# Optimization experiments

Measured on AMD Instinct MI355X. Metric: run time of the kernel, lower is better.

Reference implementation:

```python
import jax, jax.numpy as jnp
import numpy as np

N_NODES = 2000
NEG_SLOPE = 0.01  # torch nn.LeakyReLU default


def setup_inputs() -> dict:
    key = jax.random.key(0)
    ks = jax.random.split(key, 7)
    B, T, N, F, E = 4, 12, N_NODES, 64, 32000
    state = jax.random.normal(ks[0], (B, T, N, F), dtype=jnp.float32)
    feature = jax.random.normal(ks[1], (N, F), dtype=jnp.float32)
    W = jax.random.normal(ks[2], (F, 2 * F), dtype=jnp.float32) / np.sqrt(2 * F)
    b = jnp.zeros((F,), dtype=jnp.float32)
    src = jax.random.randint(ks[3], (E,), 0, N)
    dst = jax.random.randint(ks[4], (E,), 0, N)
    dist = jax.random.uniform(ks[5], (E, 1), dtype=jnp.float32)
    return {"state": state, "feature": feature, "W": W, "b": b,
            "src": src, "dst": dst, "dist": dist}


def reference(state, feature, W, b, src, dst, dist):
    # state: [B,T,N,F] -> node-major [N,B,T,F] (matches unsqueeze/transpose/squeeze)
    s = jnp.moveaxis(state, 2, 0)                       # [N,B,T,F]
    s_src = s[src]                                      # [E,B,T,F] gather
    s_dst = s[dst]                                      # [E,B,T,F]
    h = jnp.concatenate([s_src, s_dst], axis=-1)        # [E,B,T,2F]
    alpha = jnp.einsum('ebtk,fk->ebtf', h, W) + b       # linear 2F->F
    alpha = jnp.where(alpha >= 0, alpha, NEG_SLOPE * alpha)  # LeakyReLU
    alpha = alpha * dist[:, None, None, :]              # dist [E,1] broadcast
    # segment softmax over incoming edges per destination node
    n = s.shape[0]
    m = jax.ops.segment_max(alpha, dst, num_segments=n)        # [N,B,T,F]
    ex = jnp.exp(alpha - m[dst])
    denom = jax.ops.segment_sum(ex, dst, num_segments=n)       # [N,B,T,F]
    w = ex / denom[dst]                                         # [E,B,T,F]
    new_state = jax.ops.segment_sum(w * s_src, dst, num_segments=n)
    new_state = jax.nn.relu(new_state)                  # [N,B,T,F]
    return jnp.moveaxis(new_state, 0, 2)                # [B,T,N,F]
```

## Files before the change

### kernel.cpp

```cpp
#include <hip/hip_runtime.h>
#include <hip/hip_bf16.h>
#include <hip/hip_fp16.h>
#include <math.h>


#define F_DIM 64
#define LOG2E 1.442695040888963f
#define CPAD 128
#define RSTRIDE 128

typedef _Float16 f16x8 __attribute__((ext_vector_type(8)));
typedef float f32x4 __attribute__((ext_vector_type(4)));


__global__ void hist_kernel(const int* __restrict__ dst, int* __restrict__ chunk_hist,
                            int E, int N) {
    __shared__ int h[2048];
    int t = threadIdx.x, c = blockIdx.x;
    for (int i = t; i < N; i += 256) h[i] = 0;
    __syncthreads();
    int e = c * 256 + t;
    if (e < E) atomicAdd(&h[dst[e]], 1);
    __syncthreads();
    for (int d = t; d < N; d += 256)
        chunk_hist[d * CPAD + c] = h[d];
}

__global__ void binscan_kernel(int* __restrict__ chunk_hist, int* __restrict__ counts,
                               int* __restrict__ esrc, float* __restrict__ edist,
                               int N, int C) {
    int wave = (blockIdx.x * blockDim.x + threadIdx.x) >> 6;
    int lane = threadIdx.x & 63;
    if (wave >= N) return;
    int* row = chunk_hist + wave * CPAD;
    int i0 = 2 * lane, i1 = 2 * lane + 1;
    int v0 = (i0 < C) ? row[i0] : 0;
    int v1 = (i1 < C) ? row[i1] : 0;
    int s = v0 + v1;
    int acc = s;
#pragma unroll
    for (int d = 1; d < 64; d <<= 1) {
        int up = __shfl_up(acc, d);
        if (lane >= d) acc += up;
    }
    int excl = acc - s;
    if (i0 < C) row[i0] = excl;
    if (i1 < C) row[i1] = excl + v0;
    int total = __shfl(acc, 63);
    if (lane == 63) counts[wave] = total;
    int* er = esrc + wave * RSTRIDE;
    float* dr = edist + wave * RSTRIDE;
    if (i0 >= total) { er[i0] = 0; dr[i0] = 0.f; }
    if (i1 >= total) { er[i1] = 0; dr[i1] = 0.f; }
}

__global__ void scatter2_kernel(const int* __restrict__ dst, const int* __restrict__ src,
                                const float* __restrict__ dist,
                                const int* __restrict__ chunk_hist,
                                int* __restrict__ esrc, float* __restrict__ edist, int E) {
    __shared__ int sdst[256];
    int t = threadIdx.x, c = blockIdx.x;
    int e = c * 256 + t;
    int d = (e < E) ? dst[e] : -1;
    sdst[t] = d;
    __syncthreads();
    if (e >= E) return;
    int cnt = 0;
#pragma unroll 8
    for (int j = 0; j < 256; j++)
        cnt += (j < t && sdst[j] == d) ? 1 : 0;
    int off = chunk_hist[d * CPAD + c] + cnt;
    if (off < RSTRIDE) {
        esrc[d * RSTRIDE + off] = src[e] << 8;
        edist[d * RSTRIDE + off] = dist[e] * LOG2E;
    }
}

__global__ __launch_bounds__(256) void gemm_pre_mfma(
    const float* __restrict__ state, const float* __restrict__ W,
    const float* __restrict__ bias,
    unsigned* __restrict__ PSh, float* __restrict__ P2B) {
    int tid = threadIdx.x;
    int wv = tid >> 6, lane = tid & 63;
    int l15 = lane & 15, l4 = lane >> 4;

    f16x8 bf[8][2];
#pragma unroll
    for (int ct = 0; ct < 8; ++ct) {
        int j = ct * 16 + l15;
        const float* wp = (j < 64) ? (W + j * 128) : (W + (j - 64) * 128 + 64);
#pragma unroll
        for (int kh = 0; kh < 2; ++kh) {
            const float* p = wp + kh * 32 + l4 * 8;
            float4 w0 = *(const float4*)p;
            float4 w1 = *(const float4*)(p + 4);
            f16x8 h;
            h[0] = (_Float16)w0.x; h[1] = (_Float16)w0.y;
            h[2] = (_Float16)w0.z; h[3] = (_Float16)w0.w;
            h[4] = (_Float16)w1.x; h[5] = (_Float16)w1.y;
            h[6] = (_Float16)w1.z; h[7] = (_Float16)w1.w;
            bf[ct][kh] = h;
        }
    }
    float b0 = bias[l15], b1 = bias[16 + l15], b2 = bias[32 + l15], b3 = bias[48 + l15];

    int r = blockIdx.x * 64 + wv * 16;

    const float* ap = state + (long)(r + l15) * 64 + l4 * 8;
    float4 a0 = *(const float4*)ap;
    float4 a1 = *(const float4*)(ap + 4);
    float4 a2 = *(const float4*)(ap + 32);
    float4 a3 = *(const float4*)(ap + 36);
    f16x8 af0, af1;
    af0[0] = (_Float16)a0.x; af0[1] = (_Float16)a0.y;
    af0[2] = (_Float16)a0.z; af0[3] = (_Float16)a0.w;
    af0[4] = (_Float16)a1.x; af0[5] = (_Float16)a1.y;
    af0[6] = (_Float16)a1.z; af0[7] = (_Float16)a1.w;
    af1[0] = (_Float16)a2.x; af1[1] = (_Float16)a2.y;
    af1[2] = (_Float16)a2.z; af1[3] = (_Float16)a2.w;
    af1[4] = (_Float16)a3.x; af1[5] = (_Float16)a3.y;
    af1[6] = (_Float16)a3.z; af1[7] = (_Float16)a3.w;

    f32x4 zero = {0.f, 0.f, 0.f, 0.f};
    f32x4 acc[8];
#pragma unroll
    for (int ct = 0; ct < 8; ++ct) {
        acc[ct] = __builtin_amdgcn_mfma_f32_16x16x32_f16(af0, bf[ct][0], zero, 0, 0, 0);
        acc[ct] = __builtin_amdgcn_mfma_f32_16x16x32_f16(af1, bf[ct][1], acc[ct], 0, 0, 0);
    }

    float bb0[4] = {b0, b1, b2, b3};
#pragma unroll
    for (int reg = 0; reg < 4; ++reg) {
        long rr = r + l4 * 4 + reg;
        const float* sp = state + rr * 64;
#pragma unroll
        for (int ct = 0; ct < 4; ++ct) {
            float sval = sp[ct * 16 + l15];
            __half2 h = __floats2half2_rn(acc[ct][reg], sval);
            PSh[rr * 64 + ct * 16 + l15] = *(unsigned*)&h;
        }
#pragma unroll
        for (int ct = 4; ct < 8; ++ct) {
            P2B[rr * 64 + (ct - 4) * 16 + l15] = acc[ct][reg] + bb0[ct - 4];
        }
    }
}


#define ECOMP(U, D, P2V, DEN, NUM)                                        \
    {                                                                     \
        float x;                                                          \
        asm("v_fma_mix_f32 %0, %1, %2, %3 op_sel:[0,0,0] op_sel_hi:[1,0,0]" \
            : "=v"(x) : "v"(U), "v"(fone), "v"(P2V));                     \
        float y0 = x * (D);                                               \
        float y1 = 0.01f * y0;                                            \
        float y = fmaxf(y0, y1);                                          \
        float p = __builtin_amdgcn_exp2f(y);                              \
        DEN += p;                                                         \
        asm("v_fma_mix_f32 %0, %1, %2, %0 op_sel:[0,1,0] op_sel_hi:[0,1,0]" \
            : "+v"(NUM) : "v"(p), "v"(U));                                \
    }

__global__ __launch_bounds__(384) void gat_kernel(
    const unsigned* __restrict__ PSh, const float* __restrict__ P2B,
    const int* __restrict__ esrc, const float* __restrict__ edist,
    const int* __restrict__ counts,
    float* __restrict__ out, int N, int NBT) {
    int b = blockIdx.x;
    int xcd = b & 7, pr = b >> 3;
    int w = threadIdx.x >> 6, f = threadIdx.x & 63;
    int bt = xcd * 6 + w;
    const char* PSb = (const char*)PSh + (size_t)bt * N * 256;
    int f4 = f << 2;
    int n0 = pr * 2;
    int cnt0 = counts[n0], cnt1 = counts[n0 + 1];
    const int4*   ep0 = (const int4*)(esrc + n0 * RSTRIDE);
    const float4* dp0 = (const float4*)(edist + n0 * RSTRIDE);
    const int4*   ep1 = ep0 + (RSTRIDE / 4);
    const float4* dp1 = dp0 + (RSTRIDE / 4);
    int ob0 = ((bt * N + n0) << 6) + f;
    float p2_0 = P2B[ob0];
    float p2_1 = P2B[ob0 + 64];
    unsigned z = *(const unsigned*)(PSb + f4);
    float zs = __half22float2(*(const __half2*)&z).y;
    float fone = 1.0f;
    int cm0 = (cnt0 > RSTRIDE) ? RSTRIDE : cnt0;
    int cm1 = (cnt1 > RSTRIDE) ? RSTRIDE : cnt1;
    int nq0 = (cm0 + 3) >> 2, nq1 = (cm1 + 3) >> 2;
    int nqm = (nq0 > nq1) ? nq0 : nq1;
    float denA0 = 0.f, denA1 = 0.f, numA0 = 0.f, numA1 = 0.f;
    float denB0 = 0.f, denB1 = 0.f, numB0 = 0.f, numB1 = 0.f;
    for (int q = 0; q < nqm; ++q) {
        int4   sa = ep0[q], sb = ep1[q];
        float4 da = dp0[q], db = dp1[q];
        unsigned a0 = *(const unsigned*)(PSb + sa.x + f4);
        unsigned a1 = *(const unsigned*)(PSb + sa.y + f4);
        unsigned a2 = *(const unsigned*)(PSb + sa.z + f4);
        unsigned a3 = *(const unsigned*)(PSb + sa.w + f4);
        unsigned b0 = *(const unsigned*)(PSb + sb.x + f4);
        unsigned b1 = *(const unsigned*)(PSb + sb.y + f4);
        unsigned b2 = *(const unsigned*)(PSb + sb.z + f4);
        unsigned b3 = *(const unsigned*)(PSb + sb.w + f4);
        ECOMP(a0, da.x, p2_0, denA0, numA0)
        ECOMP(b0, db.x, p2_1, denB0, numB0)
        ECOMP(a1, da.y, p2_0, denA1, numA1)
        ECOMP(b1, db.y, p2_1, denB1, numB1)
        ECOMP(a2, da.z, p2_0, denA0, numA0)
        ECOMP(b2, db.z, p2_1, denB0, numB0)
        ECOMP(a3, da.w, p2_0, denA1, numA1)
        ECOMP(b3, db.w, p2_1, denB1, numB1)
    }
    float npad0 = (float)((nqm << 2) - cm0);
    float npad1 = (float)((nqm << 2) - cm1);
    float o0 = (cnt0 > 0)
        ? fmaxf((numA0 + numA1 - npad0 * zs) / (denA0 + denA1 - npad0), 0.f) : 0.f;
    float o1 = (cnt1 > 0)
        ? fmaxf((numB0 + numB1 - npad1 * zs) / (denB0 + denB1 - npad1), 0.f) : 0.f;
    out[ob0] = o0;
    out[ob0 + 64] = o1;
}


extern "C" void kernel_launch(void* const* d_in, const int* in_sizes, int n_in,
                              void* d_out, int out_size, void* d_ws, size_t ws_size,
                              hipStream_t stream) {
    const float* state = (const float*)d_in[0];
    const float* W     = (const float*)d_in[2];
    const float* bias  = (const float*)d_in[3];
    const int*   src   = (const int*)d_in[4];
    const int*   dst   = (const int*)d_in[5];
    const float* dist  = (const float*)d_in[6];
    float* out = (float*)d_out;

    int N   = in_sizes[1] / F_DIM;
    int E   = in_sizes[4];
    int NBT = in_sizes[0] / (N * F_DIM);
    int C   = (E + 255) / 256;

    size_t pelems = (size_t)NBT * N * F_DIM;
    unsigned* PSh = (unsigned*)d_ws;
    float* P2B = (float*)(PSh + pelems);
    int* counts     = (int*)(P2B + pelems);
    int* chunk_hist = counts + 2048;
    int* esrc       = chunk_hist + N * CPAD;
    float* edist    = (float*)(esrc + N * RSTRIDE);

    hist_kernel<<<C, 256, 0, stream>>>(dst, chunk_hist, E, N);
    binscan_kernel<<<(N * 64 + 255) / 256, 256, 0, stream>>>(chunk_hist, counts,
                                                             esrc, edist, N, C);
    scatter2_kernel<<<C, 256, 0, stream>>>(dst, src, dist, chunk_hist, esrc, edist, E);

    int total_rows = NBT * N;
    gemm_pre_mfma<<<total_rows / 64, 256, 0, stream>>>(state, W, bias, PSh, P2B);

    gat_kernel<<<(N / 2) * 8, 384, 0, stream>>>(PSh, P2B, esrc, edist, counts,
                                                out, N, NBT);
}
```

Baseline: 89.81 us.

## Fuse histogram into GEMM launch and handle uneven edge counts per node

```diff
diff --git a/kernel.cpp b/kernel.cpp
--- a/kernel.cpp
+++ b/kernel.cpp
@@ -12,18 +12,90 @@
 typedef _Float16 f16x8 __attribute__((ext_vector_type(8)));
 typedef float f32x4 __attribute__((ext_vector_type(4)));
 
-
-__global__ void hist_kernel(const int* __restrict__ dst, int* __restrict__ chunk_hist,
-                            int E, int N) {
+__global__ __launch_bounds__(256) void gemm_hist(
+    const float* __restrict__ state, const float* __restrict__ W,
+    const float* __restrict__ bias,
+    unsigned* __restrict__ PSh, float* __restrict__ P2B,
+    const int* __restrict__ dst, int* __restrict__ chunk_hist,
+    int E, int N, int HB) {
     __shared__ int h[2048];
-    int t = threadIdx.x, c = blockIdx.x;
-    for (int i = t; i < N; i += 256) h[i] = 0;
-    __syncthreads();
-    int e = c * 256 + t;
-    if (e < E) atomicAdd(&h[dst[e]], 1);
-    __syncthreads();
-    for (int d = t; d < N; d += 256)
-        chunk_hist[d * CPAD + c] = h[d];
+    int tid = threadIdx.x;
+    if ((int)blockIdx.x < HB) {
+        int c = blockIdx.x;
+        for (int i = tid; i < N; i += 256) h[i] = 0;
+        __syncthreads();
+        int e = c * 256 + tid;
+        if (e < E) atomicAdd(&h[dst[e]], 1);
+        __syncthreads();
+        for (int d = tid; d < N; d += 256)
+            chunk_hist[d * CPAD + c] = h[d];
+        return;
+    }
+    int gb = blockIdx.x - HB;
+    int wv = tid >> 6, lane = tid & 63;
+    int l15 = lane & 15, l4 = lane >> 4;
+
+    f16x8 bf[8][2];
+#pragma unroll
+    for (int ct = 0; ct < 8; ++ct) {
+        int j = ct * 16 + l15;
+        const float* wp = (j < 64) ? (W + j * 128) : (W + (j - 64) * 128 + 64);
+#pragma unroll
+        for (int kh = 0; kh < 2; ++kh) {
+            const float* p = wp + kh * 32 + l4 * 8;
+            float4 w0 = *(const float4*)p;
+            float4 w1 = *(const float4*)(p + 4);
+            f16x8 hh;
+            hh[0] = (_Float16)w0.x; hh[1] = (_Float16)w0.y;
+            hh[2] = (_Float16)w0.z; hh[3] = (_Float16)w0.w;
+            hh[4] = (_Float16)w1.x; hh[5] = (_Float16)w1.y;
+            hh[6] = (_Float16)w1.z; hh[7] = (_Float16)w1.w;
+            bf[ct][kh] = hh;
+        }
+    }
+    float b0 = bias[l15], b1 = bias[16 + l15], b2 = bias[32 + l15], b3 = bias[48 + l15];
+
+    int r = gb * 64 + wv * 16;
+
+    const float* ap = state + (long)(r + l15) * 64 + l4 * 8;
+    float4 a0 = *(const float4*)ap;
+    float4 a1 = *(const float4*)(ap + 4);
+    float4 a2 = *(const float4*)(ap + 32);
+    float4 a3 = *(const float4*)(ap + 36);
+    f16x8 af0, af1;
+    af0[0] = (_Float16)a0.x; af0[1] = (_Float16)a0.y;
+    af0[2] = (_Float16)a0.z; af0[3] = (_Float16)a0.w;
+    af0[4] = (_Float16)a1.x; af0[5] = (_Float16)a1.y;
+    af0[6] = (_Float16)a1.z; af0[7] = (_Float16)a1.w;
+    af1[0] = (_Float16)a2.x; af1[1] = (_Float16)a2.y;
+    af1[2] = (_Float16)a2.z; af1[3] = (_Float16)a2.w;
+    af1[4] = (_Float16)a3.x; af1[5] = (_Float16)a3.y;
+    af1[6] = (_Float16)a3.z; af1[7] = (_Float16)a3.w;
+
+    f32x4 zero = {0.f, 0.f, 0.f, 0.f};
+    f32x4 acc[8];
+#pragma unroll
+    for (int ct = 0; ct < 8; ++ct) {
+        acc[ct] = __builtin_amdgcn_mfma_f32_16x16x32_f16(af0, bf[ct][0], zero, 0, 0, 0);
+        acc[ct] = __builtin_amdgcn_mfma_f32_16x16x32_f16(af1, bf[ct][1], acc[ct], 0, 0, 0);
+    }
+
+    float bb0[4] = {b0, b1, b2, b3};
+#pragma unroll
+    for (int reg = 0; reg < 4; ++reg) {
+        long rr = r + l4 * 4 + reg;
+        const float* sp = state + rr * 64;
+#pragma unroll
+        for (int ct = 0; ct < 4; ++ct) {
+            float sval = sp[ct * 16 + l15];
+            __half2 hh = __floats2half2_rn(acc[ct][reg], sval);
+            PSh[rr * 64 + ct * 16 + l15] = *(unsigned*)&hh;
+        }
+#pragma unroll
+        for (int ct = 4; ct < 8; ++ct) {
+            P2B[rr * 64 + (ct - 4) * 16 + l15] = acc[ct][reg] + bb0[ct - 4];
+        }
+    }
 }
 
 __global__ void binscan_kernel(int* __restrict__ chunk_hist, int* __restrict__ counts,
@@ -76,77 +148,6 @@
     }
 }
 
-__global__ __launch_bounds__(256) void gemm_pre_mfma(
-    const float* __restrict__ state, const float* __restrict__ W,
-    const float* __restrict__ bias,
-    unsigned* __restrict__ PSh, float* __restrict__ P2B) {
-    int tid = threadIdx.x;
-    int wv = tid >> 6, lane = tid & 63;
-    int l15 = lane & 15, l4 = lane >> 4;
-
-    f16x8 bf[8][2];
-#pragma unroll
-    for (int ct = 0; ct < 8; ++ct) {
-        int j = ct * 16 + l15;
-        const float* wp = (j < 64) ? (W + j * 128) : (W + (j - 64) * 128 + 64);
-#pragma unroll
-        for (int kh = 0; kh < 2; ++kh) {
-            const float* p = wp + kh * 32 + l4 * 8;
-            float4 w0 = *(const float4*)p;
-            float4 w1 = *(const float4*)(p + 4);
-            f16x8 h;
-            h[0] = (_Float16)w0.x; h[1] = (_Float16)w0.y;
-            h[2] = (_Float16)w0.z; h[3] = (_Float16)w0.w;
-            h[4] = (_Float16)w1.x; h[5] = (_Float16)w1.y;
-            h[6] = (_Float16)w1.z; h[7] = (_Float16)w1.w;
-            bf[ct][kh] = h;
-        }
-    }
-    float b0 = bias[l15], b1 = bias[16 + l15], b2 = bias[32 + l15], b3 = bias[48 + l15];
-
-    int r = blockIdx.x * 64 + wv * 16;
-
-    const float* ap = state + (long)(r + l15) * 64 + l4 * 8;
-    float4 a0 = *(const float4*)ap;
-    float4 a1 = *(const float4*)(ap + 4);
-    float4 a2 = *(const float4*)(ap + 32);
-    float4 a3 = *(const float4*)(ap + 36);
-    f16x8 af0, af1;
-    af0[0] = (_Float16)a0.x; af0[1] = (_Float16)a0.y;
-    af0[2] = (_Float16)a0.z; af0[3] = (_Float16)a0.w;
-    af0[4] = (_Float16)a1.x; af0[5] = (_Float16)a1.y;
-    af0[6] = (_Float16)a1.z; af0[7] = (_Float16)a1.w;
-    af1[0] = (_Float16)a2.x; af1[1] = (_Float16)a2.y;
-    af1[2] = (_Float16)a2.z; af1[3] = (_Float16)a2.w;
-    af1[4] = (_Float16)a3.x; af1[5] = (_Float16)a3.y;
-    af1[6] = (_Float16)a3.z; af1[7] = (_Float16)a3.w;
-
-    f32x4 zero = {0.f, 0.f, 0.f, 0.f};
-    f32x4 acc[8];
-#pragma unroll
-    for (int ct = 0; ct < 8; ++ct) {
-        acc[ct] = __builtin_amdgcn_mfma_f32_16x16x32_f16(af0, bf[ct][0], zero, 0, 0, 0);
-        acc[ct] = __builtin_amdgcn_mfma_f32_16x16x32_f16(af1, bf[ct][1], acc[ct], 0, 0, 0);
-    }
-
-    float bb0[4] = {b0, b1, b2, b3};
-#pragma unroll
-    for (int reg = 0; reg < 4; ++reg) {
-        long rr = r + l4 * 4 + reg;
-        const float* sp = state + rr * 64;
-#pragma unroll
-        for (int ct = 0; ct < 4; ++ct) {
-            float sval = sp[ct * 16 + l15];
-            __half2 h = __floats2half2_rn(acc[ct][reg], sval);
-            PSh[rr * 64 + ct * 16 + l15] = *(unsigned*)&h;
-        }
-#pragma unroll
-        for (int ct = 4; ct < 8; ++ct) {
-            P2B[rr * 64 + (ct - 4) * 16 + l15] = acc[ct][reg] + bb0[ct - 4];
-        }
-    }
-}
-
 
 #define ECOMP(U, D, P2V, DEN, NUM)                                        \
     {                                                                     \
@@ -160,6 +161,20 @@
         DEN += p;                                                         \
         asm("v_fma_mix_f32 %0, %1, %2, %0 op_sel:[0,1,0] op_sel_hi:[0,1,0]" \
             : "+v"(NUM) : "v"(p), "v"(U));                                \
+    }
+
+#define G4E4(EP, DP, Q, P2V, D0, D1, M0, M1)                              \
+    {                                                                     \
+        int4   sq = (EP)[Q];                                              \
+        float4 dq = (DP)[Q];                                              \
+        unsigned q0 = *(const unsigned*)(PSb + sq.x + f4);                \
+        unsigned q1 = *(const unsigned*)(PSb + sq.y + f4);                \
+        unsigned q2 = *(const unsigned*)(PSb + sq.z + f4);                \
+        unsigned q3 = *(const unsigned*)(PSb + sq.w + f4);                \
+        ECOMP(q0, dq.x, P2V, D0, M0)                                      \
+        ECOMP(q1, dq.y, P2V, D1, M1)                                      \
+        ECOMP(q2, dq.z, P2V, D0, M0)                                      \
+        ECOMP(q3, dq.w, P2V, D1, M1)                                      \
     }
 
 __global__ __launch_bounds__(384) void gat_kernel(
@@ -188,19 +203,19 @@
     int cm0 = (cnt0 > RSTRIDE) ? RSTRIDE : cnt0;
     int cm1 = (cnt1 > RSTRIDE) ? RSTRIDE : cnt1;
     int nq0 = (cm0 + 3) >> 2, nq1 = (cm1 + 3) >> 2;
-    int nqm = (nq0 > nq1) ? nq0 : nq1;
+    int nqmin = (nq0 < nq1) ? nq0 : nq1;
     float denA0 = 0.f, denA1 = 0.f, numA0 = 0.f, numA1 = 0.f;
     float denB0 = 0.f, denB1 = 0.f, numB0 = 0.f, numB1 = 0.f;
-    for (int q = 0; q < nqm; ++q) {
+    for (int q = 0; q < nqmin; ++q) {
         int4   sa = ep0[q], sb = ep1[q];
         float4 da = dp0[q], db = dp1[q];
         unsigned a0 = *(const unsigned*)(PSb + sa.x + f4);
+        unsigned b0 = *(const unsigned*)(PSb + sb.x + f4);
         unsigned a1 = *(const unsigned*)(PSb + sa.y + f4);
+        unsigned b1 = *(const unsigned*)(PSb + sb.y + f4);
         unsigned a2 = *(const unsigned*)(PSb + sa.z + f4);
+        unsigned b2 = *(const unsigned*)(PSb + sb.z + f4);
         unsigned a3 = *(const unsigned*)(PSb + sa.w + f4);
-        unsigned b0 = *(const unsigned*)(PSb + sb.x + f4);
-        unsigned b1 = *(const unsigned*)(PSb + sb.y + f4);
-        unsigned b2 = *(const unsigned*)(PSb + sb.z + f4);
         unsigned b3 = *(const unsigned*)(PSb + sb.w + f4);
         ECOMP(a0, da.x, p2_0, denA0, numA0)
         ECOMP(b0, db.x, p2_1, denB0, numB0)
@@ -211,8 +226,12 @@
         ECOMP(a3, da.w, p2_0, denA1, numA1)
         ECOMP(b3, db.w, p2_1, denB1, numB1)
     }
-    float npad0 = (float)((nqm << 2) - cm0);
-    float npad1 = (float)((nqm << 2) - cm1);
+    for (int q = nqmin; q < nq0; ++q)
+        G4E4(ep0, dp0, q, p2_0, denA0, denA1, numA0, numA1)
+    for (int q = nqmin; q < nq1; ++q)
+        G4E4(ep1, dp1, q, p2_1, denB0, denB1, numB0, numB1)
+    float npad0 = (float)((nq0 << 2) - cm0);
+    float npad1 = (float)((nq1 << 2) - cm1);
     float o0 = (cnt0 > 0)
         ? fmaxf((numA0 + numA1 - npad0 * zs) / (denA0 + denA1 - npad0), 0.f) : 0.f;
     float o1 = (cnt1 > 0)
@@ -246,14 +265,13 @@
     int* esrc       = chunk_hist + N * CPAD;
     float* edist    = (float*)(esrc + N * RSTRIDE);
 
-    hist_kernel<<<C, 256, 0, stream>>>(dst, chunk_hist, E, N);
+    int total_rows = NBT * N;
+    gemm_hist<<<C + total_rows / 64, 256, 0, stream>>>(state, W, bias, PSh, P2B,
+                                                       dst, chunk_hist, E, N, C);
     binscan_kernel<<<(N * 64 + 255) / 256, 256, 0, stream>>>(chunk_hist, counts,
                                                              esrc, edist, N, C);
     scatter2_kernel<<<C, 256, 0, stream>>>(dst, src, dist, chunk_hist, esrc, edist, E);
 
-    int total_rows = NBT * N;
-    gemm_pre_mfma<<<total_rows / 64, 256, 0, stream>>>(state, W, bias, PSh, P2B);
-
     gat_kernel<<<(N / 2) * 8, 384, 0, stream>>>(PSh, P2B, esrc, edist, counts,
                                                 out, N, NBT);
 }
```

Result: faster. 82.23 us (-8.4%).
